# Optimization experiments

Measured on AMD Instinct MI355X. Metric: run time of the kernel, lower is better.

Reference implementation:

```python
import jax, jax.numpy as jnp
import numpy as np

ND, NG, E = 50000, 100000, 600000   # n_disease, n_gene, n_edges per direction
DIN, H, OUT = 128, 64, 64


def setup_inputs() -> dict:
    key = jax.random.key(0)
    ks = jax.random.split(key, 16)

    def w(k, i, o):
        return (jax.random.normal(k, (i, o), jnp.float32) / np.float32(np.sqrt(i)))

    return {
        "x_disease": jax.random.normal(ks[0], (ND, DIN), jnp.float32),
        "x_gene": jax.random.normal(ks[1], (NG, DIN), jnp.float32),
        "edge_src_dg": jax.random.randint(ks[2], (E,), 0, ND),
        "edge_dst_dg": jax.random.randint(ks[3], (E,), 0, NG),
        "edge_src_gd": jax.random.randint(ks[4], (E,), 0, NG),
        "edge_dst_gd": jax.random.randint(ks[5], (E,), 0, ND),
        "Wl1_dg": w(ks[6], DIN, H), "bl1_dg": jnp.zeros((H,), jnp.float32), "Wr1_dg": w(ks[7], DIN, H),
        "Wl1_gd": w(ks[8], DIN, H), "bl1_gd": jnp.zeros((H,), jnp.float32), "Wr1_gd": w(ks[9], DIN, H),
        "Wl2_dg": w(ks[10], H, OUT), "bl2_dg": jnp.zeros((OUT,), jnp.float32), "Wr2_dg": w(ks[11], H, OUT),
        "Wl2_gd": w(ks[12], H, OUT), "bl2_gd": jnp.zeros((OUT,), jnp.float32), "Wr2_gd": w(ks[13], H, OUT),
    }


def _sage(x_src, x_dst, src, dst, Wl, bl, Wr, n_dst):
    # SAGEConv (bipartite, aggr='mean'): lin_l(mean_j x_src[j]) + lin_r(x_dst)
    msg_sum = jax.ops.segment_sum(x_src[src], dst, num_segments=n_dst)   # [n_dst, d]
    cnt = jax.ops.segment_sum(jnp.ones((src.shape[0],), x_src.dtype), dst, num_segments=n_dst)
    mean = msg_sum / jnp.maximum(cnt, 1.0)[:, None]   # nodes w/o in-edges -> 0
    return mean @ Wl + bl + x_dst @ Wr


def reference(x_disease, x_gene, edge_src_dg, edge_dst_dg, edge_src_gd, edge_dst_gd,
              Wl1_dg, bl1_dg, Wr1_dg, Wl1_gd, bl1_gd, Wr1_gd,
              Wl2_dg, bl2_dg, Wr2_dg, Wl2_gd, bl2_gd, Wr2_gd):
    # layer 1: both relations read the original x_dict (HeteroConv semantics)
    g1 = _sage(x_disease, x_gene, edge_src_dg, edge_dst_dg, Wl1_dg, bl1_dg, Wr1_dg, NG)
    d1 = _sage(x_gene, x_disease, edge_src_gd, edge_dst_gd, Wl1_gd, bl1_gd, Wr1_gd, ND)
    # layer 2 (no nonlinearity in the original module)
    g2 = _sage(d1, g1, edge_src_dg, edge_dst_dg, Wl2_dg, bl2_dg, Wr2_dg, NG)
    d2 = _sage(g1, d1, edge_src_gd, edge_dst_gd, Wl2_gd, bl2_gd, Wr2_gd, ND)
    return d2, g2
```

## Files before the change

### kernel.cpp

```cpp
#include <hip/hip_runtime.h>

static constexpr int DIN = 128;
static constexpr int HID = 64;
static constexpr int BIN_SHIFT = 8;
static constexpr int CHUNK = 8192;

typedef short bf16x8 __attribute__((ext_vector_type(8)));
typedef float f32x4  __attribute__((ext_vector_type(4)));
typedef _Float16 half4 __attribute__((ext_vector_type(4)));

__device__ __forceinline__ short f2bf(float f) {
    unsigned u = __float_as_uint(f);
    unsigned r = (u + 0x7fff + ((u >> 16) & 1)) >> 16;
    return (short)r;
}
__device__ __forceinline__ float bf2f(short s) {
    return __uint_as_float(((unsigned)(unsigned short)s) << 16);
}


__global__ __launch_bounds__(256) void binhist_kernel(
    const int* __restrict__ dstA, const int* __restrict__ dstB,
    int* __restrict__ binCnt, int nE, int gA, int nbA, int nbT)
{
    __shared__ int c[1024];
    for (int b = threadIdx.x; b < 1024; b += 256) c[b] = 0;
    __syncthreads();
    const int blk = blockIdx.x;
    const bool isA = blk < gA;
    const int* dst = isA ? dstA : dstB;
    const int off  = isA ? 0 : nbA;
    const int i0   = (isA ? blk : blk - gA) * CHUNK;
    #pragma unroll 4
    for (int k = 0; k < CHUNK / 256; ++k) {
        int i = i0 + k * 256 + threadIdx.x;
        if (i < nE) atomicAdd(&c[off + (dst[i] >> BIN_SHIFT)], 1);
    }
    __syncthreads();
    for (int b = threadIdx.x; b < nbT; b += 256) {
        int v = c[b];
        if (v) atomicAdd(&binCnt[b], v);
    }
}

__global__ __launch_bounds__(1024) void binscan_kernel(
    const int* __restrict__ binCnt, int* __restrict__ binBase,
    int* __restrict__ binCur, int nbT)
{
    __shared__ int s[1024];
    int v = (threadIdx.x < nbT) ? binCnt[threadIdx.x] : 0;
    s[threadIdx.x] = v;
    __syncthreads();
    for (int o = 1; o < 1024; o <<= 1) {
        int t = (threadIdx.x >= o) ? s[threadIdx.x - o] : 0;
        __syncthreads();
        s[threadIdx.x] += t;
        __syncthreads();
    }
    if (threadIdx.x < nbT) {
        binBase[threadIdx.x] = s[threadIdx.x] - v;
        binCur[threadIdx.x]  = s[threadIdx.x] - v;
    }
}

__global__ __launch_bounds__(256) void binplaceA_kernel(
    const int* __restrict__ srcA, const int* __restrict__ dstA,
    const int* __restrict__ srcB, const int* __restrict__ dstB,
    int* __restrict__ binCur, int2* __restrict__ pairs,
    int nE, int gA, int nbA, int nbT)
{
    __shared__ int cnt[1024];
    __shared__ int base[1024];
    for (int b = threadIdx.x; b < 1024; b += 256) cnt[b] = 0;
    __syncthreads();
    const int blk = blockIdx.x;
    const bool isA = blk < gA;
    const int* src = isA ? srcA : srcB;
    const int* dst = isA ? dstA : dstB;
    const int off  = isA ? 0 : nbA;
    const int i0   = (isA ? blk : blk - gA) * CHUNK;
    #pragma unroll 4
    for (int k = 0; k < CHUNK / 256; ++k) {
        int i = i0 + k * 256 + threadIdx.x;
        if (i < nE) atomicAdd(&cnt[off + (dst[i] >> BIN_SHIFT)], 1);
    }
    __syncthreads();
    for (int b = threadIdx.x; b < nbT; b += 256) {
        int v = cnt[b];
        base[b] = v ? atomicAdd(&binCur[b], v) : 0;
        cnt[b] = 0;
    }
    __syncthreads();
    #pragma unroll 4
    for (int k = 0; k < CHUNK / 256; ++k) {
        int i = i0 + k * 256 + threadIdx.x;
        if (i < nE) {
            int d  = dst[i];
            int bn = off + (d >> BIN_SHIFT);
            int p  = base[bn] + atomicAdd(&cnt[bn], 1);
            pairs[p] = make_int2(src[i], d);
        }
    }
}

__global__ __launch_bounds__(256) void binplaceB_kernel(
    const int2* __restrict__ pairs,
    const int* __restrict__ binBase, const int* __restrict__ binCnt,
    int* __restrict__ startsA, int* __restrict__ cntA, int* __restrict__ colA, int NA,
    int* __restrict__ startsB, int* __restrict__ cntB, int* __restrict__ colB, int NB,
    int nbA, int nE)
{
    __shared__ int lc[256];
    __shared__ int pr[256];
    const int b    = blockIdx.x;
    const bool isA = b < nbA;
    int* starts = isA ? startsA : startsB;
    int* cntN   = isA ? cntA : cntB;
    int* col    = isA ? colA : colB;
    const int N     = isA ? NA : NB;
    const int node0 = (isA ? b : b - nbA) << BIN_SHIFT;
    const int e0 = binBase[b];
    const int ec = binCnt[b];
    const int colBase = isA ? e0 : e0 - nE;

    lc[threadIdx.x] = 0;
    __syncthreads();
    for (int e = threadIdx.x; e < ec; e += 256)
        atomicAdd(&lc[pairs[e0 + e].y - node0], 1);
    __syncthreads();
    const int v = lc[threadIdx.x];
    pr[threadIdx.x] = v;
    __syncthreads();
    for (int o = 1; o < 256; o <<= 1) {
        int t = (threadIdx.x >= o) ? pr[threadIdx.x - o] : 0;
        __syncthreads();
        pr[threadIdx.x] += t;
        __syncthreads();
    }
    const int myStart = colBase + pr[threadIdx.x] - v;
    const int n = node0 + threadIdx.x;
    if (n < N) { starts[n] = myStart; cntN[n] = v; }
    __syncthreads();
    lc[threadIdx.x] = myStart;
    __syncthreads();
    for (int e = threadIdx.x; e < ec; e += 256) {
        int2 pd = pairs[e0 + e];
        int p = atomicAdd(&lc[pd.y - node0], 1);
        col[p] = pd.x;
    }
}

struct PackW {
    const float* Wa[4]; const float* Wb[4];
    short* oh[4]; short* ol[4];
    int K[4];
};

__global__ __launch_bounds__(256) void pack_w(PackW p) {
    const int c = blockIdx.y;
    const int K = p.K[c];
    const int t = blockIdx.x * 256 + threadIdx.x;
    if (t >= K * 16) return;
    const int f  = t >> 6, l = t & 63;
    const int ks = f >> 3, cf = f & 7;
    const int col = cf * 16 + (l & 15);
    const int kb  = ks * 32 + ((l >> 4) * 8);
    const float* s = (col < 64) ? (p.Wa[c] + col) : (p.Wb[c] + (col - 64));
    short* oh = p.oh[c] + (size_t)t * 8;
    short* ol = p.ol[c] + (size_t)t * 8;
    #pragma unroll
    for (int i = 0; i < 8; ++i) {
        float v = s[(kb + i) * 64];
        short h = f2bf(v);
        oh[i] = h;
        ol[i] = f2bf(v - bf2f(h));
    }
}

struct ProjJob {
    const float* x; const short* WH; const short* WL;
    _Float16* Pa; float* Pb; int N;
};

template<int K>
__device__ __forceinline__ void proj_body(const ProjJob& j, int bid)
{
    constexpr int NKS = K / 32;
    const int tid = threadIdx.x;
    const int l   = tid & 63;
    const int w   = tid >> 6;
    const int lr  = l & 15;
    const int lg  = l >> 4;
    const int r0  = bid * 64 + w * 16;
    const int row = r0 + lr;

    float4 u[NKS][2];
    {
        const bool ok = row < j.N;
        const float* xp = &j.x[(long long)row * K + lg * 8];
        #pragma unroll
        for (int ks = 0; ks < NKS; ++ks) {
            u[ks][0] = ok ? *(const float4*)(xp + ks * 32)     : make_float4(0.f,0.f,0.f,0.f);
            u[ks][1] = ok ? *(const float4*)(xp + ks * 32 + 4) : make_float4(0.f,0.f,0.f,0.f);
        }
    }

    f32x4 acc[8];
    #pragma unroll
    for (int c = 0; c < 8; ++c) acc[c] = (f32x4){0.f, 0.f, 0.f, 0.f};

    #pragma unroll
    for (int ks = 0; ks < NKS; ++ks) {
        bf16x8 ah, al;
        {
            const float vv[8] = {u[ks][0].x, u[ks][0].y, u[ks][0].z, u[ks][0].w,
                                 u[ks][1].x, u[ks][1].y, u[ks][1].z, u[ks][1].w};
            #pragma unroll
            for (int i = 0; i < 8; ++i) {
                short h = f2bf(vv[i]);
                ah[i] = h;
                al[i] = f2bf(vv[i] - bf2f(h));
            }
        }
        const short* wb = j.WH + (size_t)(ks * 8) * 512 + l * 8;
        const short* lb = j.WL + (size_t)(ks * 8) * 512 + l * 8;
        #pragma unroll
        for (int cf = 0; cf < 8; ++cf) {
            const bf16x8 bh = *(const bf16x8*)(wb + cf * 512);
            const bf16x8 bl = *(const bf16x8*)(lb + cf * 512);
            acc[cf] = __builtin_amdgcn_mfma_f32_16x16x32_bf16(ah, bh, acc[cf], 0, 0, 0);
            acc[cf] = __builtin_amdgcn_mfma_f32_16x16x32_bf16(ah, bl, acc[cf], 0, 0, 0);
            acc[cf] = __builtin_amdgcn_mfma_f32_16x16x32_bf16(al, bh, acc[cf], 0, 0, 0);
        }
    }

    #pragma unroll
    for (int q = 0; q < 4; ++q) {
        const int ro = r0 + lg * 4 + q;
        if (ro < j.N) {
            #pragma unroll
            for (int cf = 0; cf < 8; ++cf) {
                const float v = acc[cf][q];
                if (cf < 4) j.Pa[(long long)ro * 64 + cf * 16 + lr] = (_Float16)v;
                else        j.Pb[(long long)ro * 64 + (cf - 4) * 16 + lr] = v;
            }
        }
    }
}

template<int K>
__global__ __launch_bounds__(256) void proj_mfma2(ProjJob a, ProjJob b, int blocksA)
{
    const bool isA = (int)blockIdx.x < blocksA;
    const ProjJob j = isA ? a : b;
    const int bid = isA ? blockIdx.x : blockIdx.x - blocksA;
    proj_body<K>(j, bid);
}

struct GatherJob {
    const _Float16* P; const int* starts; const int* cnt; const int* col;
    const float* bias; float* out; int N;
};

__global__ __launch_bounds__(256) void gather2(GatherJob A, GatherJob B, int blocksA)
{
    const bool isA = (int)blockIdx.x < blocksA;
    const GatherJob g = isA ? A : B;
    const int bid = isA ? blockIdx.x : blockIdx.x - blocksA;

    const int lane = threadIdx.x & 63;
    const int wid  = (bid * 256 + threadIdx.x) >> 6;
    const int n    = wid * 4 + (lane >> 4);
    const int li   = lane & 15;
    if (n >= g.N) return;

    int e         = g.starts[n];
    const int deg = g.cnt[n];
    const int e1  = e + deg;

    float4 acc = make_float4(0.f, 0.f, 0.f, 0.f);
    while (e + 4 <= e1) {
        const int s0 = g.col[e], s1 = g.col[e + 1], s2 = g.col[e + 2], s3 = g.col[e + 3];
        const half4 v0 = *(const half4*)(g.P + (size_t)s0 * 64 + li * 4);
        const half4 v1 = *(const half4*)(g.P + (size_t)s1 * 64 + li * 4);
        const half4 v2 = *(const half4*)(g.P + (size_t)s2 * 64 + li * 4);
        const half4 v3 = *(const half4*)(g.P + (size_t)s3 * 64 + li * 4);
        acc.x += (float)v0[0] + (float)v1[0] + (float)v2[0] + (float)v3[0];
        acc.y += (float)v0[1] + (float)v1[1] + (float)v2[1] + (float)v3[1];
        acc.z += (float)v0[2] + (float)v1[2] + (float)v2[2] + (float)v3[2];
        acc.w += (float)v0[3] + (float)v1[3] + (float)v2[3] + (float)v3[3];
        e += 4;
    }
    while (e < e1) {
        const half4 v0 = *(const half4*)(g.P + (size_t)g.col[e] * 64 + li * 4);
        acc.x += (float)v0[0]; acc.y += (float)v0[1];
        acc.z += (float)v0[2]; acc.w += (float)v0[3];
        ++e;
    }
    const float inv = (deg > 0) ? 1.0f / (float)deg : 0.0f;
    const int c0 = li * 4;
    const float4 b4 = *(const float4*)&g.bias[c0];
    float4 cur = *(float4*)&g.out[(long long)n * 64 + c0];
    cur.x += acc.x * inv + b4.x;
    cur.y += acc.y * inv + b4.y;
    cur.z += acc.z * inv + b4.z;
    cur.w += acc.w * inv + b4.w;
    *(float4*)&g.out[(long long)n * 64 + c0] = cur;
}

extern "C" void kernel_launch(void* const* d_in, const int* in_sizes, int n_in,
                              void* d_out, int out_size, void* d_ws, size_t ws_size,
                              hipStream_t stream) {
    const float* x_d    = (const float*)d_in[0];
    const float* x_g    = (const float*)d_in[1];
    const int* src_dg   = (const int*)d_in[2];
    const int* dst_dg   = (const int*)d_in[3];
    const int* src_gd   = (const int*)d_in[4];
    const int* dst_gd   = (const int*)d_in[5];
    const float* Wl1_dg = (const float*)d_in[6];
    const float* bl1_dg = (const float*)d_in[7];
    const float* Wr1_dg = (const float*)d_in[8];
    const float* Wl1_gd = (const float*)d_in[9];
    const float* bl1_gd = (const float*)d_in[10];
    const float* Wr1_gd = (const float*)d_in[11];
    const float* Wl2_dg = (const float*)d_in[12];
    const float* bl2_dg = (const float*)d_in[13];
    const float* Wr2_dg = (const float*)d_in[14];
    const float* Wl2_gd = (const float*)d_in[15];
    const float* bl2_gd = (const float*)d_in[16];
    const float* Wr2_gd = (const float*)d_in[17];

    const int nd = in_sizes[0] / DIN;
    const int ng = in_sizes[1] / DIN;
    const int ne = in_sizes[2];

    _Float16* P_d = (_Float16*)d_ws;
    _Float16* P_g = P_d + (size_t)nd * HID;
    int* startsG = (int*)(P_g + (size_t)ng * HID);
    int* startsD = startsG + ng;
    int* cntG    = startsD + nd;
    int* cntD    = cntG + ng;
    int* colG    = cntD + nd;
    int* colD    = colG + ne;
    int* binCnt  = colD + ne;
    int* binBase = binCnt + 1024;
    int* binCur  = binBase + 1024;

    uintptr_t pp = (uintptr_t)(binCur + 1024);
    pp = (pp + 15) & ~(uintptr_t)15;
    int2* pairs = (int2*)pp;

    uintptr_t wp = (uintptr_t)(pairs + 2 * (size_t)ne);
    wp = (wp + 63) & ~(uintptr_t)63;
    short* wh0 = (short*)wp;
    short* wl0 = wh0 + 16384;
    short* wh1 = wl0 + 16384;
    short* wl1 = wh1 + 16384;
    short* wh2 = wl1 + 16384;
    short* wl2 = wh2 + 8192;
    short* wh3 = wl2 + 8192;
    short* wl3 = wh3 + 8192;

    float* out  = (float*)d_out;
    float* d1r  = out;
    float* g1r  = out + (size_t)nd * HID;

    const int gBH = (ne + CHUNK - 1) / CHUNK;
    const int nbG = (ng + 255) >> 8;
    const int nbD = (nd + 255) >> 8;
    const int nbT = nbG + nbD;
    const int gM_g = (ng + 63) / 64;
    const int gM_d = (nd + 63) / 64;
    const int gG_g = (ng + 15) / 16;
    const int gG_d = (nd + 15) / 16;

    PackW pw;
    pw.Wa[0] = Wl1_dg; pw.Wb[0] = Wr1_gd; pw.oh[0] = wh0; pw.ol[0] = wl0; pw.K[0] = 128;
    pw.Wa[1] = Wl1_gd; pw.Wb[1] = Wr1_dg; pw.oh[1] = wh1; pw.ol[1] = wl1; pw.K[1] = 128;
    pw.Wa[2] = Wl2_gd; pw.Wb[2] = Wr2_dg; pw.oh[2] = wh2; pw.ol[2] = wl2; pw.K[2] = 64;
    pw.Wa[3] = Wl2_dg; pw.Wb[3] = Wr2_gd; pw.oh[3] = wh3; pw.ol[3] = wl3; pw.K[3] = 64;
    pack_w<<<dim3(8, 4), 256, 0, stream>>>(pw);

    hipMemsetAsync(binCnt, 0, 1024 * sizeof(int), stream);

    binhist_kernel<<<2 * gBH, 256, 0, stream>>>(dst_dg, dst_gd, binCnt, ne, gBH, nbG, nbT);
    binscan_kernel<<<1, 1024, 0, stream>>>(binCnt, binBase, binCur, nbT);
    binplaceA_kernel<<<2 * gBH, 256, 0, stream>>>(src_dg, dst_dg, src_gd, dst_gd,
                                                  binCur, pairs, ne, gBH, nbG, nbT);
    binplaceB_kernel<<<nbT, 256, 0, stream>>>(pairs, binBase, binCnt,
                                              startsG, cntG, colG, ng,
                                              startsD, cntD, colD, nd, nbG, ne);

    ProjJob p1a = { x_d, wh0, wl0, P_d, d1r, nd };
    ProjJob p1b = { x_g, wh1, wl1, P_g, g1r, ng };
    proj_mfma2<DIN><<<gM_d + gM_g, 256, 0, stream>>>(p1a, p1b, gM_d);

    GatherJob ga1 = { P_d, startsG, cntG, colG, bl1_dg, g1r, ng };
    GatherJob gb1 = { P_g, startsD, cntD, colD, bl1_gd, d1r, nd };
    gather2<<<gG_g + gG_d, 256, 0, stream>>>(ga1, gb1, gG_g);

    ProjJob p2a = { g1r, wh2, wl2, P_g, g1r, ng };
    ProjJob p2b = { d1r, wh3, wl3, P_d, d1r, nd };
    proj_mfma2<HID><<<gM_g + gM_d, 256, 0, stream>>>(p2a, p2b, gM_g);

    GatherJob ga2 = { P_g, startsD, cntD, colD, bl2_gd, d1r, nd };
    GatherJob gb2 = { P_d, startsG, cntG, colG, bl2_dg, g1r, ng };
    gather2<<<gG_d + gG_g, 256, 0, stream>>>(ga2, gb2, gG_d);
}
```

Measured before the change: 341.3 us.

## Stage projection weights in LDS and coalesce output stores via shared memory

The projection kernel now copies the split bf16 weight matrices (hi/lo) into shared memory once per block and feeds the MFMAs from LDS instead of global memory. The accumulator results are also staged through padded LDS tiles and written out as 16-byte vector stores per row, replacing scattered 2-byte and 4-byte stores. This targets repeated global weight reads and uncoalesced epilogue writes. In exchange it uses 64KB of LDS per block, which may limit occupancy, and adds block-wide barriers.

Result: faster. 327.1 us (-4.2%).

```diff
diff --git a/kernel.cpp b/kernel.cpp
--- a/kernel.cpp
+++ b/kernel.cpp
@@ -8,6 +8,7 @@
 typedef short bf16x8 __attribute__((ext_vector_type(8)));
 typedef float f32x4  __attribute__((ext_vector_type(4)));
 typedef _Float16 half4 __attribute__((ext_vector_type(4)));
+typedef _Float16 half8 __attribute__((ext_vector_type(8)));
 
 __device__ __forceinline__ short f2bf(float f) {
     unsigned u = __float_as_uint(f);
@@ -17,7 +18,6 @@
 __device__ __forceinline__ float bf2f(short s) {
     return __uint_as_float(((unsigned)(unsigned short)s) << 16);
 }
-
 
 __global__ __launch_bounds__(256) void binhist_kernel(
     const int* __restrict__ dstA, const int* __restrict__ dstB,
@@ -182,10 +182,21 @@
     _Float16* Pa; float* Pb; int N;
 };
 
+static constexpr int PA_LD = 72;
+static constexpr int PB_LD = 68;
+
 template<int K>
-__device__ __forceinline__ void proj_body(const ProjJob& j, int bid)
+__global__ __launch_bounds__(256) void proj_mfma2(ProjJob a, ProjJob b, int blocksA)
 {
     constexpr int NKS = K / 32;
+    __shared__ short sWbuf[32768];
+    short* sWH = sWbuf;
+    short* sWL = sWbuf + K * 128;
+
+    const bool isA = (int)blockIdx.x < blocksA;
+    const ProjJob j = isA ? a : b;
+    const int bid = isA ? blockIdx.x : blockIdx.x - blocksA;
+
     const int tid = threadIdx.x;
     const int l   = tid & 63;
     const int w   = tid >> 6;
@@ -193,6 +204,11 @@
     const int lg  = l >> 4;
     const int r0  = bid * 64 + w * 16;
     const int row = r0 + lr;
+
+    for (int t = tid; t < K * 16; t += 256) {
+        *(bf16x8*)(sWH + t * 8) = *(const bf16x8*)(j.WH + t * 8);
+        *(bf16x8*)(sWL + t * 8) = *(const bf16x8*)(j.WL + t * 8);
+    }
 
     float4 u[NKS][2];
     {
@@ -204,6 +220,7 @@
             u[ks][1] = ok ? *(const float4*)(xp + ks * 32 + 4) : make_float4(0.f,0.f,0.f,0.f);
         }
     }
+    __syncthreads();
 
     f32x4 acc[8];
     #pragma unroll
@@ -222,8 +239,8 @@
                 al[i] = f2bf(vv[i] - bf2f(h));
             }
         }
-        const short* wb = j.WH + (size_t)(ks * 8) * 512 + l * 8;
-        const short* lb = j.WL + (size_t)(ks * 8) * 512 + l * 8;
+        const short* wb = sWH + (ks * 8) * 512 + l * 8;
+        const short* lb = sWL + (ks * 8) * 512 + l * 8;
         #pragma unroll
         for (int cf = 0; cf < 8; ++cf) {
             const bf16x8 bh = *(const bf16x8*)(wb + cf * 512);
@@ -234,27 +251,34 @@
         }
     }
 
+    __syncthreads();
+    _Float16* sPa = (_Float16*)sWbuf;
+    float*    sPb = (float*)(sWbuf + 64 * PA_LD);
+
     #pragma unroll
     for (int q = 0; q < 4; ++q) {
-        const int ro = r0 + lg * 4 + q;
-        if (ro < j.N) {
-            #pragma unroll
-            for (int cf = 0; cf < 8; ++cf) {
-                const float v = acc[cf][q];
-                if (cf < 4) j.Pa[(long long)ro * 64 + cf * 16 + lr] = (_Float16)v;
-                else        j.Pb[(long long)ro * 64 + (cf - 4) * 16 + lr] = v;
-            }
+        const int r = w * 16 + lg * 4 + q;
+        #pragma unroll
+        for (int cf = 0; cf < 8; ++cf) {
+            const float v = acc[cf][q];
+            if (cf < 4) sPa[r * PA_LD + cf * 16 + lr] = (_Float16)v;
+            else        sPb[r * PB_LD + (cf - 4) * 16 + lr] = v;
         }
     }
-}
-
-template<int K>
-__global__ __launch_bounds__(256) void proj_mfma2(ProjJob a, ProjJob b, int blocksA)
-{
-    const bool isA = (int)blockIdx.x < blocksA;
-    const ProjJob j = isA ? a : b;
-    const int bid = isA ? blockIdx.x : blockIdx.x - blocksA;
-    proj_body<K>(j, bid);
+    __syncthreads();
+
+    for (int c = tid; c < 512; c += 256) {
+        const int r = c >> 3, cc = (c & 7) * 8;
+        const int gr = bid * 64 + r;
+        if (gr < j.N)
+            *(half8*)(j.Pa + (size_t)gr * 64 + cc) = *(half8*)(sPa + r * PA_LD + cc);
+    }
+    for (int c = tid; c < 1024; c += 256) {
+        const int r = c >> 4, cc = (c & 15) * 4;
+        const int gr = bid * 64 + r;
+        if (gr < j.N)
+            *(float4*)(j.Pb + (size_t)gr * 64 + cc) = *(float4*)(sPb + r * PB_LD + cc);
+    }
 }
 
 struct GatherJob {
```
